# Kernel optimization log

Measured on AMD Instinct MI355X. Metric: run time of the kernel, lower is better.

Reference implementation:

```python
import jax, jax.numpy as jnp
import numpy as np

H = 2048
K_SRC = (H * H) // 4  # exact nonzero count of mask_src (fixed in setup_inputs)
K_TAR = (H * H) // 4  # exact nonzero count of mask_tar
NBINS = 256


def de_norm(x):
    return jnp.clip((x + 1.0) / 2.0, 0.0, 1.0)


def cal_hist_cdf(vals):
    # vals: [3, K] float in [0, 255]. torch.histc(bins=256, min=0, max=256)
    # has unit-width bins -> bin index = floor(v). Returns cumulative pdf [3, 256].
    idx = jnp.clip(vals.astype(jnp.int32), 0, NBINS - 1)
    flat = (idx + jnp.arange(3, dtype=jnp.int32)[:, None] * NBINS).ravel()
    hist = jnp.bincount(flat, length=3 * NBINS).reshape(3, NBINS).astype(vals.dtype)
    pdf = hist / hist.sum(axis=1, keepdims=True)
    return jnp.cumsum(pdf, axis=1)


def cal_trans(dst_cdf, ref_cdf):
    # Faithful to PSGAN cal_trans(ref=dst_cdf, adj=ref_cdf):
    # table[i] = first j in [1,255] with ref_cdf[j-1] <= dst_cdf[i] <= ref_cdf[j],
    # else i; table[255] = 255. First valid j equals searchsorted-left (clipped).
    i = jnp.arange(NBINS)
    j = jnp.clip(jnp.searchsorted(ref_cdf, dst_cdf, side='left'), 1, NBINS - 1)
    valid = (ref_cdf[j - 1] <= dst_cdf) & (dst_cdf <= ref_cdf[j])
    table = jnp.where(valid, j, i)
    return table.at[NBINS - 1].set(NBINS - 1)


def setup_inputs():
    key = jax.random.key(0)
    k1, k2 = jax.random.split(key)
    rng = np.random.default_rng(0)

    def make_mask(K):
        m = np.zeros(H * H, np.float32)
        m[rng.permutation(H * H)[:K]] = 1.0
        return jnp.asarray(m.reshape(1, 1, H, H))

    return {
        "input_data": jax.random.normal(k1, (1, 3, H, H), jnp.float32),
        "target_data": jax.random.normal(k2, (1, 3, H, H), jnp.float32),
        "mask_src": make_mask(K_SRC),
        "mask_tar": make_mask(K_TAR),
    }


def reference(input_data, target_data, mask_src, mask_tar):
    m_src = mask_src[0, 0]  # [H, H]
    m_tar = mask_tar[0, 0]
    # nonzero() returns row-major (y, x) index pairs, same as torch
    ys, xs = jnp.nonzero(m_src, size=K_SRC)
    yt, xt = jnp.nonzero(m_tar, size=K_TAR)

    inp = de_norm(input_data)[0] * 255.0   # [3, H, H]
    tar = de_norm(target_data)[0] * 255.0
    input_masked = inp * m_src[None]
    target_masked = tar * m_tar[None]

    dst_align = input_masked[:, ys, xs]    # [3, K_SRC]
    ref_align = target_masked[:, yt, xt]   # [3, K_TAR]

    cdf_dst = cal_hist_cdf(dst_align)
    cdf_ref = cal_hist_cdf(ref_align)
    tables = jax.vmap(cal_trans)(cdf_dst, cdf_ref)  # [3, 256]

    # remap: tables[c][int(dst_align[c,k])] (int() truncation, values >= 0)
    bins = jnp.clip(dst_align.astype(jnp.int32), 0, NBINS - 1)
    mapped = jnp.take_along_axis(tables, bins, axis=1).astype(input_masked.dtype)

    # scatter matched values back into the masked input image; detached in torch
    input_match = jax.lax.stop_gradient(input_masked.at[:, ys, xs].set(mapped))
    return jnp.mean(jnp.abs(input_masked - input_match))
```

## Files before the change

kernel.cpp:

```cpp
#include <hip/hip_runtime.h>
#include <hip/hip_bf16.h>

#define HDIM 2048
#define HH (HDIM * HDIM)
#define NBINS 256
#define KCNT 1048576.0f
#define TOTAL_ELEMS 12582912.0

#define ROW_DWORDS 2304
#define ROW_BYTES  9216
#define TAIL_BYTES (6 * NBINS * sizeof(int) + 3 * NBINS * sizeof(double))
#define ROWS_PER_CHUNK 32

__device__ __forceinline__ float de_norm255(float x) {
    float v = (x + 1.0f) * 0.5f;
    v = fminf(fmaxf(v, 0.0f), 1.0f) * 255.0f;
    return v;
}

__global__ void hist_kernel(const float* __restrict__ inp,
                            const float* __restrict__ tar,
                            const float* __restrict__ msrc,
                            const float* __restrict__ mtar,
                            int* __restrict__ parts) {
    __shared__ int   lcnt[6 * NBINS];
    __shared__ float lsum[3 * NBINS];
    for (int i = threadIdx.x; i < 6 * NBINS; i += blockDim.x) lcnt[i] = 0;
    for (int i = threadIdx.x; i < 3 * NBINS; i += blockDim.x) lsum[i] = 0.0f;
    __syncthreads();

    int nz[6] = {0, 0, 0, 0, 0, 0};
    int nf[6] = {0, 0, 0, 0, 0, 0};

    const int stride = gridDim.x * blockDim.x;
    const int n4 = HH / 4;
    for (int p4 = blockIdx.x * blockDim.x + threadIdx.x; p4 < n4; p4 += stride) {
        float4 ms4 = ((const float4*)msrc)[p4];
        float4 mt4 = ((const float4*)mtar)[p4];
        float m[4] = {ms4.x, ms4.y, ms4.z, ms4.w};
        float t[4] = {mt4.x, mt4.y, mt4.z, mt4.w};
        #pragma unroll
        for (int c = 0; c < 3; ++c) {
            float4 v4 = ((const float4*)(inp + (size_t)c * HH))[p4];
            float4 w4 = ((const float4*)(tar + (size_t)c * HH))[p4];
            float vv[4] = {v4.x, v4.y, v4.z, v4.w};
            float ww[4] = {w4.x, w4.y, w4.z, w4.w};
            #pragma unroll
            for (int k = 0; k < 4; ++k) {
                if (m[k] != 0.0f) {
                    float v = de_norm255(vv[k]);
                    if (v == 0.0f)         nz[c]++;
                    else if (v == 255.0f)  nf[c]++;
                    else {
                        int b = (int)v;
                        atomicAdd(&lcnt[c * NBINS + b], 1);
                        atomicAdd(&lsum[c * NBINS + b], v);
                    }
                }
                if (t[k] != 0.0f) {
                    float v = de_norm255(ww[k]);
                    if (v == 0.0f)         nz[3 + c]++;
                    else if (v == 255.0f)  nf[3 + c]++;
                    else {
                        int b = (int)v;
                        atomicAdd(&lcnt[(3 + c) * NBINS + b], 1);
                    }
                }
            }
        }
    }

    #pragma unroll
    for (int j = 0; j < 6; ++j) {
        int a = nz[j], f = nf[j];
        #pragma unroll
        for (int off = 32; off > 0; off >>= 1) {
            a += __shfl_down(a, off, 64);
            f += __shfl_down(f, off, 64);
        }
        if ((threadIdx.x & 63) == 0) {
            if (a) atomicAdd(&lcnt[j * NBINS + 0], a);
            if (f) atomicAdd(&lcnt[j * NBINS + NBINS - 1], f);
        }
    }
    __syncthreads();

    int* row = parts + (size_t)blockIdx.x * ROW_DWORDS;
    for (int i = threadIdx.x; i < ROW_DWORDS; i += blockDim.x)
        row[i] = (i < 6 * NBINS) ? lcnt[i] : __float_as_int(lsum[i - 6 * NBINS]);
}

__global__ void reduce_kernel(const int* __restrict__ parts, int nblk,
                              int* __restrict__ counts,
                              double* __restrict__ sums) {
    const int j = blockIdx.x * blockDim.x + threadIdx.x;
    if (j >= ROW_DWORDS) return;
    int w0 = blockIdx.y * ROWS_PER_CHUNK;
    int w1 = w0 + ROWS_PER_CHUNK;
    if (w1 > nblk) w1 = nblk;
    if (w0 >= w1) return;

    if (j < 6 * NBINS) {
        int acc = 0;
        for (int w = w0; w < w1; ++w) acc += parts[(size_t)w * ROW_DWORDS + j];
        if (acc) atomicAdd(&counts[j], acc);
    } else {
        double acc = 0.0;
        for (int w = w0; w < w1; ++w)
            acc += (double)__int_as_float(parts[(size_t)w * ROW_DWORDS + j]);
        if (acc != 0.0) atomicAdd(&sums[j - 6 * NBINS], acc);
    }
}

__global__ void final_kernel(const int* __restrict__ counts,
                             const double* __restrict__ sums,
                             float* __restrict__ out) {
    __shared__ float cdf[6][NBINS];
    __shared__ int   lcnt[6 * NBINS];
    __shared__ double red[12];
    const int tid = threadIdx.x;
    lcnt[tid]       = counts[tid];
    lcnt[tid + 768] = counts[tid + 768];
    __syncthreads();

    if (tid < 6) {
        float run = 0.0f;
        for (int i = 0; i < NBINS; ++i) {
            run += (float)lcnt[tid * NBINS + i] * (1.0f / KCNT);
            cdf[tid][i] = run;
        }
    }
    __syncthreads();

    const int c = tid >> 8, b = tid & (NBINS - 1);
    const float d = cdf[c][b];
    const float* r = cdf[3 + c];
    int lo = 0, hi = NBINS;
    while (lo < hi) {
        int mid = (lo + hi) >> 1;
        if (r[mid] < d) lo = mid + 1; else hi = mid;
    }
    int j = lo;
    if (j < 1) j = 1;
    if (j > NBINS - 1) j = NBINS - 1;
    bool valid = (r[j - 1] <= d) && (d <= r[j]);
    int t = valid ? j : b;
    if (b == NBINS - 1) t = NBINS - 1;

    const int n = lcnt[c * NBINS + b];
    const double s = (b == NBINS - 1) ? 255.0 * (double)n : sums[c * NBINS + b];
    double contrib = (t <= b) ? (s - (double)n * (double)t)
                              : ((double)n * (double)t - s);

    #pragma unroll
    for (int off = 32; off > 0; off >>= 1)
        contrib += __shfl_down(contrib, off, 64);
    const int wave = tid >> 6, lane = tid & 63;
    if (lane == 0) red[wave] = contrib;
    __syncthreads();
    if (tid == 0) {
        double tot = 0.0;
        for (int w = 0; w < 12; ++w) tot += red[w];
        out[0] = (float)(tot / TOTAL_ELEMS);
    }
}

extern "C" void kernel_launch(void* const* d_in, const int* in_sizes, int n_in,
                              void* d_out, int out_size, void* d_ws, size_t ws_size,
                              hipStream_t stream) {
    const float* inp  = (const float*)d_in[0];
    const float* tar  = (const float*)d_in[1];
    const float* msrc = (const float*)d_in[2];
    const float* mtar = (const float*)d_in[3];
    float* out = (float*)d_out;

    int nblk = 1024;
    if (ws_size < (size_t)nblk * ROW_BYTES + TAIL_BYTES) {
        size_t avail = ws_size > TAIL_BYTES ? (ws_size - TAIL_BYTES) / ROW_BYTES : 1;
        nblk = avail < 1 ? 1 : (int)avail;
    }

    char* ws = (char*)d_ws;
    int*    parts  = (int*)ws;
    int*    counts = (int*)(ws + (size_t)nblk * ROW_BYTES);
    double* sums   = (double*)(ws + (size_t)nblk * ROW_BYTES + 6 * NBINS * sizeof(int));

    hipMemsetAsync((void*)counts, 0, TAIL_BYTES, stream);

    const int nchunks = (nblk + ROWS_PER_CHUNK - 1) / ROWS_PER_CHUNK;
    dim3 rgrid((ROW_DWORDS + 255) / 256, nchunks);

    hist_kernel<<<nblk, 256, 0, stream>>>(inp, tar, msrc, mtar, parts);
    reduce_kernel<<<rgrid, 256, 0, stream>>>(parts, nblk, counts, sums);
    final_kernel<<<1, 3 * NBINS, 0, stream>>>(counts, sums, out);
}
```

Baseline: 52.42 us.

## Pack count and fixed-point fraction into single 64-bit LDS atomic per sample

Replaces the separate int count atomic and float sum atomic for the source histogram with a single 64-bit atomic that packs the count in the high bits and a fixed-point fractional part in the low bits. Atomics become branchless: masked-out lanes hit a per-lane dummy slot, which avoids divergent branches. The reduce and final kernels are adapted to unpack counts and fractions, and the grid doubles to 2048 blocks. The trade-off is that every lane now issues atomics, including masked ones, and fixed-point fraction precision is limited.

```diff
diff --git a/kernel.cpp b/kernel.cpp
--- a/kernel.cpp
+++ b/kernel.cpp
@@ -7,9 +7,13 @@
 #define KCNT 1048576.0f
 #define TOTAL_ELEMS 12582912.0
 
-#define ROW_DWORDS 2304
+#define FRAC_SCALE 33554432.0f
+#define FRAC_INV   (1.0 / 33554432.0)
+#define FRAC_MASK  ((1ull << 40) - 1)
+
+#define ROW_U64    1152
 #define ROW_BYTES  9216
-#define TAIL_BYTES (6 * NBINS * sizeof(int) + 3 * NBINS * sizeof(double))
+#define TAIL_BYTES (1536 * sizeof(int) + 768 * sizeof(unsigned long long))
 #define ROWS_PER_CHUNK 32
 
 __device__ __forceinline__ float de_norm255(float x) {
@@ -22,12 +26,19 @@
                             const float* __restrict__ tar,
                             const float* __restrict__ msrc,
                             const float* __restrict__ mtar,
-                            int* __restrict__ parts) {
-    __shared__ int   lcnt[6 * NBINS];
-    __shared__ float lsum[3 * NBINS];
-    for (int i = threadIdx.x; i < 6 * NBINS; i += blockDim.x) lcnt[i] = 0;
-    for (int i = threadIdx.x; i < 3 * NBINS; i += blockDim.x) lsum[i] = 0.0f;
-    __syncthreads();
+                            unsigned long long* __restrict__ parts) {
+    __shared__ unsigned long long h64[3 * NBINS];
+    __shared__ unsigned long long dummy64[64];
+    __shared__ unsigned int       h32[3 * NBINS];
+    for (int i = threadIdx.x; i < 3 * NBINS; i += blockDim.x) {
+        h64[i] = 0ull;
+        h32[i] = 0u;
+    }
+    if (threadIdx.x < 64) dummy64[threadIdx.x] = 0ull;
+    __syncthreads();
+
+    const int lane = threadIdx.x & 63;
+    unsigned long long* const dslot = &dummy64[lane];
 
     int nz[6] = {0, 0, 0, 0, 0, 0};
     int nf[6] = {0, 0, 0, 0, 0, 0};
@@ -47,24 +58,28 @@
             float ww[4] = {w4.x, w4.y, w4.z, w4.w};
             #pragma unroll
             for (int k = 0; k < 4; ++k) {
-                if (m[k] != 0.0f) {
+                {
+                    const bool on = (m[k] != 0.0f);
                     float v = de_norm255(vv[k]);
-                    if (v == 0.0f)         nz[c]++;
-                    else if (v == 255.0f)  nf[c]++;
-                    else {
-                        int b = (int)v;
-                        atomicAdd(&lcnt[c * NBINS + b], 1);
-                        atomicAdd(&lsum[c * NBINS + b], v);
-                    }
+                    int b = (int)v;
+                    float frac = v - (float)b;
+                    unsigned fx = (unsigned)(frac * FRAC_SCALE);
+                    const bool mid = on & (v > 0.0f) & (v < 255.0f);
+                    unsigned long long* addr = mid ? &h64[c * NBINS + b] : dslot;
+                    atomicAdd(addr, (1ull << 40) | (unsigned long long)fx);
+                    nz[c] += (int)(on & (v == 0.0f));
+                    nf[c] += (int)(on & (v == 255.0f));
                 }
-                if (t[k] != 0.0f) {
-                    float v = de_norm255(ww[k]);
-                    if (v == 0.0f)         nz[3 + c]++;
-                    else if (v == 255.0f)  nf[3 + c]++;
-                    else {
-                        int b = (int)v;
-                        atomicAdd(&lcnt[(3 + c) * NBINS + b], 1);
-                    }
+                {
+                    const bool on = (t[k] != 0.0f);
+                    float w = de_norm255(ww[k]);
+                    int b = (int)w;
+                    const bool mid = on & (w > 0.0f) & (w < 255.0f);
+                    unsigned int* addr = mid ? &h32[c * NBINS + b]
+                                             : (unsigned int*)dslot;
+                    atomicAdd(addr, 1u);
+                    nz[3 + c] += (int)(on & (w == 0.0f));
+                    nf[3 + c] += (int)(on & (w == 255.0f));
                 }
             }
         }
@@ -78,42 +93,60 @@
             a += __shfl_down(a, off, 64);
             f += __shfl_down(f, off, 64);
         }
-        if ((threadIdx.x & 63) == 0) {
-            if (a) atomicAdd(&lcnt[j * NBINS + 0], a);
-            if (f) atomicAdd(&lcnt[j * NBINS + NBINS - 1], f);
-        }
-    }
-    __syncthreads();
-
-    int* row = parts + (size_t)blockIdx.x * ROW_DWORDS;
-    for (int i = threadIdx.x; i < ROW_DWORDS; i += blockDim.x)
-        row[i] = (i < 6 * NBINS) ? lcnt[i] : __float_as_int(lsum[i - 6 * NBINS]);
-}
-
-__global__ void reduce_kernel(const int* __restrict__ parts, int nblk,
+        if (lane == 0) {
+            if (j < 3) {
+                if (a) atomicAdd(&h64[j * NBINS + 0],
+                                 ((unsigned long long)a) << 40);
+                if (f) atomicAdd(&h64[j * NBINS + NBINS - 1],
+                                 ((unsigned long long)f) << 40);
+            } else {
+                if (a) atomicAdd(&h32[(j - 3) * NBINS + 0], (unsigned)a);
+                if (f) atomicAdd(&h32[(j - 3) * NBINS + NBINS - 1], (unsigned)f);
+            }
+        }
+    }
+    __syncthreads();
+
+    unsigned long long* row64 = parts + (size_t)blockIdx.x * ROW_U64;
+    for (int i = threadIdx.x; i < 3 * NBINS; i += blockDim.x)
+        row64[i] = h64[i];
+    unsigned int* row32 = (unsigned int*)(row64 + 3 * NBINS);
+    for (int i = threadIdx.x; i < 3 * NBINS; i += blockDim.x)
+        row32[i] = h32[i];
+}
+
+__global__ void reduce_kernel(const unsigned long long* __restrict__ parts,
+                              int nblk,
                               int* __restrict__ counts,
-                              double* __restrict__ sums) {
+                              unsigned long long* __restrict__ fracs) {
     const int j = blockIdx.x * blockDim.x + threadIdx.x;
-    if (j >= ROW_DWORDS) return;
+    if (j >= 1536) return;
     int w0 = blockIdx.y * ROWS_PER_CHUNK;
     int w1 = w0 + ROWS_PER_CHUNK;
     if (w1 > nblk) w1 = nblk;
     if (w0 >= w1) return;
 
-    if (j < 6 * NBINS) {
-        int acc = 0;
-        for (int w = w0; w < w1; ++w) acc += parts[(size_t)w * ROW_DWORDS + j];
-        if (acc) atomicAdd(&counts[j], acc);
+    if (j < 768) {
+        unsigned long long cnt = 0, fr = 0;
+        for (int w = w0; w < w1; ++w) {
+            unsigned long long p = parts[(size_t)w * ROW_U64 + j];
+            cnt += p >> 40;
+            fr  += p & FRAC_MASK;
+        }
+        if (cnt) atomicAdd(&counts[j], (int)cnt);
+        if (fr)  atomicAdd(&fracs[j], fr);
     } else {
-        double acc = 0.0;
+        const unsigned int* p32 = (const unsigned int*)parts;
+        int cnt = 0;
+        const int jj = j - 768;
         for (int w = w0; w < w1; ++w)
-            acc += (double)__int_as_float(parts[(size_t)w * ROW_DWORDS + j]);
-        if (acc != 0.0) atomicAdd(&sums[j - 6 * NBINS], acc);
+            cnt += p32[(size_t)w * (2 * ROW_U64) + 1536 + jj];
+        if (cnt) atomicAdd(&counts[768 + jj], cnt);
     }
 }
 
 __global__ void final_kernel(const int* __restrict__ counts,
-                             const double* __restrict__ sums,
+                             const unsigned long long* __restrict__ fracs,
                              float* __restrict__ out) {
     __shared__ float cdf[6][NBINS];
     __shared__ int   lcnt[6 * NBINS];
@@ -148,7 +181,8 @@
     if (b == NBINS - 1) t = NBINS - 1;
 
     const int n = lcnt[c * NBINS + b];
-    const double s = (b == NBINS - 1) ? 255.0 * (double)n : sums[c * NBINS + b];
+    const double s = (double)n * (double)b
+                   + (double)(long long)fracs[c * NBINS + b] * FRAC_INV;
     double contrib = (t <= b) ? (s - (double)n * (double)t)
                               : ((double)n * (double)t - s);
 
@@ -174,23 +208,25 @@
     const float* mtar = (const float*)d_in[3];
     float* out = (float*)d_out;
 
-    int nblk = 1024;
+    int nblk = 2048;
     if (ws_size < (size_t)nblk * ROW_BYTES + TAIL_BYTES) {
         size_t avail = ws_size > TAIL_BYTES ? (ws_size - TAIL_BYTES) / ROW_BYTES : 1;
-        nblk = avail < 1 ? 1 : (int)avail;
+        nblk = avail < 256 ? 256 : (int)avail;
+        if (nblk > 2048) nblk = 2048;
     }
 
     char* ws = (char*)d_ws;
-    int*    parts  = (int*)ws;
-    int*    counts = (int*)(ws + (size_t)nblk * ROW_BYTES);
-    double* sums   = (double*)(ws + (size_t)nblk * ROW_BYTES + 6 * NBINS * sizeof(int));
+    unsigned long long* parts = (unsigned long long*)ws;
+    int*                counts = (int*)(ws + (size_t)nblk * ROW_BYTES);
+    unsigned long long* fracs  = (unsigned long long*)(ws + (size_t)nblk * ROW_BYTES
+                                                          + 1536 * sizeof(int));
 
     hipMemsetAsync((void*)counts, 0, TAIL_BYTES, stream);
 
     const int nchunks = (nblk + ROWS_PER_CHUNK - 1) / ROWS_PER_CHUNK;
-    dim3 rgrid((ROW_DWORDS + 255) / 256, nchunks);
+    dim3 rgrid(6, nchunks);
 
     hist_kernel<<<nblk, 256, 0, stream>>>(inp, tar, msrc, mtar, parts);
-    reduce_kernel<<<rgrid, 256, 0, stream>>>(parts, nblk, counts, sums);
-    final_kernel<<<1, 3 * NBINS, 0, stream>>>(counts, sums, out);
-}
+    reduce_kernel<<<rgrid, 256, 0, stream>>>(parts, nblk, counts, fracs);
+    final_kernel<<<1, 3 * NBINS, 0, stream>>>(counts, fracs, out);
+}
```

After: 55.35 us. +5.6%, slower.
